# Performance work log

Measured on AMD Instinct MI355X. Metric: run time of the kernel, lower is better.

Reference implementation:

```python
import jax, jax.numpy as jnp
import numpy as np

D_CONV = 4  # matches Mamba(d_conv=4)


def _silu(v):
    return v * jax.nn.sigmoid(v)


def _mamba_block(x, in_w, cw, cb, xw, dtw, dtb, A_log, Dp, ow):
    # x: (B, L, d_model)
    B, L, _ = x.shape
    d_inner, d_state = A_log.shape
    xz = x @ in_w.T                        # (B, L, 2*d_inner)
    xr, z = jnp.split(xz, 2, axis=-1)      # each (B, L, d_inner)
    # causal depthwise conv1d (pad d_conv-1 on the left, truncate to L)
    xp = jnp.pad(xr, ((0, 0), (D_CONV - 1, 0), (0, 0)))
    xc = sum(xp[:, k:k + L, :] * cw[:, k] for k in range(D_CONV)) + cb
    xc = _silu(xc)                         # (B, L, d_inner)
    dbl = xc @ xw.T                        # (B, L, dt_rank + 2*d_state)
    dt_rank = dbl.shape[-1] - 2 * d_state
    dt, Bm, Cm = jnp.split(dbl, [dt_rank, dt_rank + d_state], axis=-1)
    dt = jax.nn.softplus(dt @ dtw.T + dtb)  # (B, L, d_inner)
    A = -jnp.exp(A_log)                    # (d_inner, d_state)
    dA = jnp.exp(dt[..., None] * A)                          # (B, L, d_inner, d_state)
    dBx = dt[..., None] * Bm[:, :, None, :] * xc[..., None]  # (B, L, d_inner, d_state)

    def step(h, inputs):
        dA_t, dBx_t, C_t = inputs          # (B,d,s), (B,d,s), (B,s)
        h = dA_t * h + dBx_t
        y = jnp.einsum('bds,bs->bd', h, C_t)
        return h, y

    h0 = jnp.zeros((B, d_inner, d_state), x.dtype)
    _, ys = jax.lax.scan(step, h0, (dA.transpose(1, 0, 2, 3),
                                    dBx.transpose(1, 0, 2, 3),
                                    Cm.transpose(1, 0, 2)))
    y = ys.transpose(1, 0, 2) + xc * Dp    # skip term D*u
    y = y * _silu(z)                       # gated
    return y @ ow.T                        # (B, L, d_model)


def setup_inputs() -> dict:
    key = jax.random.key(0)
    d_model, d_state, n_layer = 1024, 16, 2
    d_inner = 2 * d_model
    dt_rank = d_model // 16  # ceil(1024/16)
    Bsz, L = 2, 1024
    ks = jax.random.split(key, 8)
    s = 0.02
    x = jax.random.normal(ks[0], (Bsz, L, d_model), jnp.float32)
    in_proj_w = jax.random.normal(ks[1], (n_layer, 2 * d_inner, d_model), jnp.float32) * s
    conv_w = jax.random.normal(ks[2], (n_layer, d_inner, D_CONV), jnp.float32) * 0.2
    conv_b = jnp.zeros((n_layer, d_inner), jnp.float32)
    x_proj_w = jax.random.normal(ks[3], (n_layer, dt_rank + 2 * d_state, d_inner), jnp.float32) * s
    dt_proj_w = jax.random.normal(ks[4], (n_layer, d_inner, dt_rank), jnp.float32) * s
    dt_proj_b = jax.random.uniform(ks[5], (n_layer, d_inner), jnp.float32, -5.0, -3.0)
    A_log = jnp.log(jnp.tile(jnp.arange(1, d_state + 1, dtype=jnp.float32), (n_layer, d_inner, 1)))
    D = jnp.ones((n_layer, d_inner), jnp.float32)
    out_proj_w = jax.random.normal(ks[6], (n_layer, d_model, d_inner), jnp.float32) * s
    return {"x": x, "in_proj_w": in_proj_w, "conv_w": conv_w, "conv_b": conv_b,
            "x_proj_w": x_proj_w, "dt_proj_w": dt_proj_w, "dt_proj_b": dt_proj_b,
            "A_log": A_log, "D": D, "out_proj_w": out_proj_w}


def reference(x, in_proj_w, conv_w, conv_b, x_proj_w, dt_proj_w, dt_proj_b, A_log, D, out_proj_w):
    n_layer = in_proj_w.shape[0]
    for i in range(n_layer):
        x = _mamba_block(x, in_proj_w[i], conv_w[i], conv_b[i], x_proj_w[i],
                         dt_proj_w[i], dt_proj_b[i], A_log[i], D[i], out_proj_w[i])
    return x
```

## Files before the change

### kernel.cpp

```cpp
#include <hip/hip_runtime.h>
#include <hip/hip_bf16.h>
#include <cmath>

typedef __bf16 bf16x8_t __attribute__((ext_vector_type(8)));
typedef float  f32x4_t  __attribute__((ext_vector_type(4)));
using bf16 = __hip_bfloat16;

#define LOG2E 1.44269504088896340736f
#define LN2   0.69314718055994530942f

#define AS1C(p) ((const __attribute__((address_space(1))) void*)(p))
#define AS3C(p) ((__attribute__((address_space(3))) void*)(p))

__device__ __forceinline__ float fexp2(float x) { return __builtin_amdgcn_exp2f(x); }
__device__ __forceinline__ float flog2(float x) { return __builtin_amdgcn_logf(x); }
__device__ __forceinline__ float frcp (float x) { return __builtin_amdgcn_rcpf(x); }

__global__ __launch_bounds__(256)
void cast_f32_bf16(const float* __restrict__ src, bf16* __restrict__ dst, int n8)
{
    const int i = blockIdx.x * blockDim.x + threadIdx.x;
    if (i >= n8) return;
    const float4* s = (const float4*)(src + (size_t)i * 8);
    float4 a = s[0], b = s[1];
    bf16 o[8];
    o[0] = __float2bfloat16(a.x); o[1] = __float2bfloat16(a.y);
    o[2] = __float2bfloat16(a.z); o[3] = __float2bfloat16(a.w);
    o[4] = __float2bfloat16(b.x); o[5] = __float2bfloat16(b.y);
    o[6] = __float2bfloat16(b.z); o[7] = __float2bfloat16(b.w);
    *(int4*)(dst + (size_t)i * 8) = *(int4*)o;
}

template<int MODE, bool SPLITK>
__global__ __launch_bounds__(256)
void gemm_bf16(const bf16* __restrict__ A, const bf16* __restrict__ B,
               float* __restrict__ Cf, bf16* __restrict__ Cb,
               int M, int N, int K, int lda, int ldb, int ldc)
{
    __shared__ __align__(16) bf16 At[2][128][32];
    __shared__ __align__(16) bf16 Bt[2][128][32];

    const int tid  = threadIdx.x;
    const int lane = tid & 63;
    const int wid  = tid >> 6;
    const int wr   = wid >> 1;
    const int wc   = wid & 1;
    const int fr   = lane & 15;
    const int fq   = lane >> 4;

    const int row0 = blockIdx.y * 128;
    const int col0 = blockIdx.x * 128;
    const int kb   = SPLITK ? blockIdx.z * K : 0;

    const int g_row = wid * 32 + (lane >> 2);
    const int g_kp  = (lane & 3) * 8;
    const bf16* aP0 = A + (size_t)(row0 + g_row) * lda + g_kp + kb;
    const bf16* aP1 = A + (size_t)(row0 + g_row + 16) * lda + g_kp + kb;
    int bR0 = col0 + g_row;      if (bR0 >= N) bR0 = N - 1;
    int bR1 = col0 + g_row + 16; if (bR1 >= N) bR1 = N - 1;
    const bf16* bP0 = B + (size_t)bR0 * ldb + g_kp + kb;
    const bf16* bP1 = B + (size_t)bR1 * ldb + g_kp + kb;

    f32x4_t acc[4][4];
    #pragma unroll
    for (int m = 0; m < 4; ++m)
        #pragma unroll
        for (int n = 0; n < 4; ++n)
            acc[m][n] = f32x4_t{0.f, 0.f, 0.f, 0.f};

    auto STAGE = [&](int buf, int k0) {
        __builtin_amdgcn_global_load_lds(AS1C(aP0 + k0), AS3C(&At[buf][wid * 32][0]),      16, 0, 0);
        __builtin_amdgcn_global_load_lds(AS1C(aP1 + k0), AS3C(&At[buf][wid * 32 + 16][0]), 16, 0, 0);
        __builtin_amdgcn_global_load_lds(AS1C(bP0 + k0), AS3C(&Bt[buf][wid * 32][0]),      16, 0, 0);
        __builtin_amdgcn_global_load_lds(AS1C(bP1 + k0), AS3C(&Bt[buf][wid * 32 + 16][0]), 16, 0, 0);
    };

    STAGE(0, 0);
    __syncthreads();
    int cur = 0;
    for (int k0 = 0; k0 < K; k0 += 32) {
        if (k0 + 32 < K) STAGE(cur ^ 1, k0 + 32);

        bf16x8_t af[4], bg[4];
        #pragma unroll
        for (int m = 0; m < 4; ++m)
            af[m] = *(const bf16x8_t*)&At[cur][wr * 64 + m * 16 + fr][fq * 8];
        #pragma unroll
        for (int n = 0; n < 4; ++n)
            bg[n] = *(const bf16x8_t*)&Bt[cur][wc * 64 + n * 16 + fr][fq * 8];
        #pragma unroll
        for (int m = 0; m < 4; ++m)
            #pragma unroll
            for (int n = 0; n < 4; ++n)
                acc[m][n] = __builtin_amdgcn_mfma_f32_16x16x32_bf16(
                    af[m], bg[n], acc[m][n], 0, 0, 0);

        __syncthreads();
        cur ^= 1;
    }

    float* Cfz = SPLITK ? (Cf + (size_t)blockIdx.z * M * ldc) : Cf;

    #pragma unroll
    for (int m = 0; m < 4; ++m) {
        #pragma unroll
        for (int n = 0; n < 4; ++n) {
            const int c = col0 + wc * 64 + n * 16 + fr;
            if (c < N) {
                #pragma unroll
                for (int r = 0; r < 4; ++r) {
                    const int rr = row0 + wr * 64 + m * 16 + fq * 4 + r;
                    if (SPLITK || MODE != 1) Cfz[(size_t)rr * ldc + c] = acc[m][n][r];
                    if (!SPLITK && MODE != 0) Cb[(size_t)rr * ldc + c] = __float2bfloat16(acc[m][n][r]);
                }
            }
        }
    }
}

__global__ __launch_bounds__(256)
void reduce_pk(const float* __restrict__ part, float* __restrict__ of,
               bf16* __restrict__ oh, int n4, int stride4, int S)
{
    const int i = blockIdx.x * blockDim.x + threadIdx.x;
    if (i >= n4) return;
    const float4* p4 = (const float4*)part;
    float4 s = p4[i];
    for (int k = 1; k < S; ++k) {
        float4 v = p4[(size_t)k * stride4 + i];
        s.x += v.x; s.y += v.y; s.z += v.z; s.w += v.w;
    }
    if (of) ((float4*)of)[i] = s;
    if (oh) {
        bf16 o[4];
        o[0] = __float2bfloat16(s.x); o[1] = __float2bfloat16(s.y);
        o[2] = __float2bfloat16(s.z); o[3] = __float2bfloat16(s.w);
        *(int2*)(oh + (size_t)i * 4) = *(int2*)o;
    }
}

__global__ __launch_bounds__(256)
void conv_silu(const float* __restrict__ xz, const float* __restrict__ cw,
               const float* __restrict__ cb, bf16* __restrict__ xc,
               int Bsz, int L, int dinner)
{
    const int nv = dinner / 4;
    const int g  = blockIdx.x * blockDim.x + threadIdx.x;
    const int d4 = (g % nv) * 4;
    const int t  = (g / nv) % L;
    const int b  = g / (nv * L);
    if (b >= Bsz) return;

    const int ldxz = 2 * dinner;
    float4 w0 = *(const float4*)(cw + (size_t)(d4 + 0) * 4);
    float4 w1 = *(const float4*)(cw + (size_t)(d4 + 1) * 4);
    float4 w2 = *(const float4*)(cw + (size_t)(d4 + 2) * 4);
    float4 w3 = *(const float4*)(cw + (size_t)(d4 + 3) * 4);
    float4 acc = *(const float4*)(cb + d4);

    const float* base = xz + (size_t)b * L * ldxz + d4;
    #pragma unroll
    for (int k = 0; k < 4; ++k) {
        const int ts = t - 3 + k;
        if (ts >= 0) {
            float4 v = *(const float4*)(base + (size_t)ts * ldxz);
            acc.x = fmaf(v.x, (&w0.x)[k], acc.x);
            acc.y = fmaf(v.y, (&w1.x)[k], acc.y);
            acc.z = fmaf(v.z, (&w2.x)[k], acc.z);
            acc.w = fmaf(v.w, (&w3.x)[k], acc.w);
        }
    }
    acc.x = acc.x * frcp(1.f + fexp2(-acc.x * LOG2E));
    acc.y = acc.y * frcp(1.f + fexp2(-acc.y * LOG2E));
    acc.z = acc.z * frcp(1.f + fexp2(-acc.z * LOG2E));
    acc.w = acc.w * frcp(1.f + fexp2(-acc.w * LOG2E));

    bf16 o[4];
    o[0] = __float2bfloat16(acc.x); o[1] = __float2bfloat16(acc.y);
    o[2] = __float2bfloat16(acc.z); o[3] = __float2bfloat16(acc.w);
    *(int2*)(xc + ((size_t)b * L + t) * dinner + d4) = *(int2*)o;
}

__global__ __launch_bounds__(256)
void scan_part1(const bf16* __restrict__ dtraw, const bf16* __restrict__ xc,
                const float* __restrict__ dbl, const float* __restrict__ dtb,
                const float* __restrict__ alog, float* __restrict__ hend,
                float* __restrict__ Ssum, int Bsz, int L, int dinner,
                int NC, int CL)
{
    const int g  = blockIdx.x * blockDim.x + threadIdx.x;
    const int sq = g & 3;
    const int d  = (g >> 2) % dinner;
    const int c  = ((g >> 2) / dinner) % NC;
    const int b  = g / (4 * dinner * NC);
    if (b >= Bsz) return;

    float4 av = *(const float4*)(alog + (size_t)d * 16 + sq * 4);
    const float As0 = -fexp2(av.x * LOG2E) * LOG2E;
    const float As1 = -fexp2(av.y * LOG2E) * LOG2E;
    const float As2 = -fexp2(av.z * LOG2E) * LOG2E;
    const float As3 = -fexp2(av.w * LOG2E) * LOG2E;
    const float bias = dtb[d];

    const int t0 = c * CL;
    const bf16*  dt_p = dtraw + ((size_t)b * L + t0) * dinner + d;
    const bf16*  xc_p = xc    + ((size_t)b * L + t0) * dinner + d;
    const float* bl_p = dbl   + ((size_t)b * L + t0) * 96 + 64 + sq * 4;

    float h0 = 0.f, h1 = 0.f, h2 = 0.f, h3 = 0.f, S = 0.f;
    for (int t = 0; t < CL; ++t) {
        const float dtv = __bfloat162float(*dt_p);
        const float xcv = __bfloat162float(*xc_p);
        const float4 Bv = *(const float4*)bl_p;

        const float xv = dtv + bias;
        const float e  = fexp2(xv * LOG2E);
        const float sp = (xv > 15.f) ? xv : LN2 * flog2(1.f + e);
        S += sp;
        const float u = sp * xcv;
        h0 = fmaf(fexp2(sp * As0), h0, u * Bv.x);
        h1 = fmaf(fexp2(sp * As1), h1, u * Bv.y);
        h2 = fmaf(fexp2(sp * As2), h2, u * Bv.z);
        h3 = fmaf(fexp2(sp * As3), h3, u * Bv.w);

        dt_p += dinner; xc_p += dinner; bl_p += 96;
    }

    const size_t idx = ((size_t)b * NC + c) * dinner + d;
    *(float4*)(hend + idx * 16 + sq * 4) = make_float4(h0, h1, h2, h3);
    if (sq == 0) Ssum[idx] = S;
}

__global__ __launch_bounds__(256)
void chunk_prefix(float* __restrict__ hend, const float* __restrict__ Ssum,
                  const float* __restrict__ alog, int Bsz, int dinner, int NC)
{
    const int g = blockIdx.x * blockDim.x + threadIdx.x;
    const int s = g & 15;
    const int d = (g >> 4) % dinner;
    const int b = g / (16 * dinner);
    if (b >= Bsz) return;

    const float As2 = -fexp2(alog[(size_t)d * 16 + s] * LOG2E) * LOG2E;

    float h = 0.f;
    for (int c = 0; c < NC; ++c) {
        const size_t idx = ((size_t)b * NC + c) * dinner + d;
        const float he = hend[idx * 16 + s];
        const float Sv = Ssum[idx];
        hend[idx * 16 + s] = h;
        h = fmaf(fexp2(As2 * Sv), h, he);
    }
}

__global__ __launch_bounds__(256)
void scan_part2(bf16* dty, const bf16* __restrict__ xc,
                const float* __restrict__ dbl, const float* __restrict__ xz,
                const float* __restrict__ dtb, const float* __restrict__ alog,
                const float* __restrict__ Dp, const float* __restrict__ hinit,
                int Bsz, int L, int dinner, int NC, int CL)
{
    const int g  = blockIdx.x * blockDim.x + threadIdx.x;
    const int sq = g & 3;
    const int d  = (g >> 2) % dinner;
    const int c  = ((g >> 2) / dinner) % NC;
    const int b  = g / (4 * dinner * NC);
    if (b >= Bsz) return;

    float4 av = *(const float4*)(alog + (size_t)d * 16 + sq * 4);
    const float As0 = -fexp2(av.x * LOG2E) * LOG2E;
    const float As1 = -fexp2(av.y * LOG2E) * LOG2E;
    const float As2 = -fexp2(av.z * LOG2E) * LOG2E;
    const float As3 = -fexp2(av.w * LOG2E) * LOG2E;
    const float bias = dtb[d];
    const float Dval = Dp[d];

    const size_t cidx = ((size_t)b * NC + c) * dinner + d;
    float4 hv = *(const float4*)(hinit + cidx * 16 + sq * 4);
    float h0 = hv.x, h1 = hv.y, h2 = hv.z, h3 = hv.w;

    const int t0 = c * CL;
    bf16*        dt_p = dty + ((size_t)b * L + t0) * dinner + d;
    const bf16*  xc_p = xc  + ((size_t)b * L + t0) * dinner + d;
    const float* bl_p = dbl + ((size_t)b * L + t0) * 96 + 64 + sq * 4;
    const float* z_p  = xz  + ((size_t)b * L + t0) * (2 * dinner) + dinner + d;

    for (int t = 0; t < CL; ++t) {
        const float dtv = __bfloat162float(*dt_p);
        const float xcv = __bfloat162float(*xc_p);
        const float4 Bv = *(const float4*)bl_p;
        const float4 Cv = *(const float4*)(bl_p + 16);
        const float zv  = *z_p;

        const float xv = dtv + bias;
        const float e  = fexp2(xv * LOG2E);
        const float sp = (xv > 15.f) ? xv : LN2 * flog2(1.f + e);
        const float u = sp * xcv;
        h0 = fmaf(fexp2(sp * As0), h0, u * Bv.x);
        h1 = fmaf(fexp2(sp * As1), h1, u * Bv.y);
        h2 = fmaf(fexp2(sp * As2), h2, u * Bv.z);
        h3 = fmaf(fexp2(sp * As3), h3, u * Bv.w);

        float y = h0 * Cv.x + h1 * Cv.y + h2 * Cv.z + h3 * Cv.w;
        y += __shfl_xor(y, 1, 4);
        y += __shfl_xor(y, 2, 4);

        if (sq == 0) {
            y = fmaf(xcv, Dval, y);
            const float sig = frcp(1.f + fexp2(-zv * LOG2E));
            *dt_p = __float2bfloat16(y * (zv * sig));
        }

        dt_p += dinner; xc_p += dinner; bl_p += 96; z_p += 2 * dinner;
    }
}

extern "C" void kernel_launch(void* const* d_in, const int* in_sizes, int n_in,
                              void* d_out, int out_size, void* d_ws, size_t ws_size,
                              hipStream_t stream)
{
    const float* x    = (const float*)d_in[0];
    const float* inw  = (const float*)d_in[1];
    const float* cw   = (const float*)d_in[2];
    const float* cb   = (const float*)d_in[3];
    const float* xw   = (const float*)d_in[4];
    const float* dtw  = (const float*)d_in[5];
    const float* dtb  = (const float*)d_in[6];
    const float* alog = (const float*)d_in[7];
    const float* Dp   = (const float*)d_in[8];
    const float* ow   = (const float*)d_in[9];
    float* out = (float*)d_out;

    const int Bsz = 2, L = 1024, dmodel = 1024, dinner = 2048;
    const int BL = Bsz * L;
    const int NC = 32, CL = L / NC;
    const int SPX = 8,  KSX = dinner / SPX;
    const int SPO = 2,  KSO = dinner / SPO;

    char* p = (char*)d_ws;
    auto alloc = [&](size_t bytes) { char* r = p; p += (bytes + 63) & ~size_t(63); return r; };
    bf16*  wb_in  = (bf16*) alloc((size_t)2 * 2 * dinner * dmodel * 2);
    bf16*  wb_x   = (bf16*) alloc((size_t)2 * 96 * dinner * 2);
    bf16*  wb_dt  = (bf16*) alloc((size_t)2 * dinner * 64 * 2);
    bf16*  wb_ow  = (bf16*) alloc((size_t)2 * dmodel * dinner * 2);
    bf16*  curb   = (bf16*) alloc((size_t)BL * dmodel * 2);
    float* xzb    = (float*)alloc((size_t)BL * 2 * dinner * 4);
    bf16*  xcb16  = (bf16*) alloc((size_t)BL * dinner * 2);
    float* dblb   = (float*)alloc((size_t)BL * 96 * 4);
    bf16*  dblb16 = (bf16*) alloc((size_t)BL * 96 * 2);
    bf16*  dtrb16 = (bf16*) alloc((size_t)BL * dinner * 2);
    float* hendb  = (float*)alloc((size_t)Bsz * NC * dinner * 16 * 4);
    float* ssumb  = (float*)alloc((size_t)Bsz * NC * dinner * 4);
    float* partb  = (float*)alloc((size_t)SPO * BL * dmodel * 4);

    const int scan_blocks = (Bsz * NC * dinner * 4) / 256;
    const int pfx_blocks  = (Bsz * dinner * 16) / 256;

    cast_f32_bf16<<<(BL * dmodel / 8) / 256, 256, 0, stream>>>(x, curb, BL * dmodel / 8);
    cast_f32_bf16<<<(2 * 2 * dinner * dmodel / 8) / 256, 256, 0, stream>>>(
        inw, wb_in, 2 * 2 * dinner * dmodel / 8);
    cast_f32_bf16<<<(2 * 96 * dinner / 8) / 256, 256, 0, stream>>>(
        xw, wb_x, 2 * 96 * dinner / 8);
    cast_f32_bf16<<<(2 * dinner * 64 / 8) / 256, 256, 0, stream>>>(
        dtw, wb_dt, 2 * dinner * 64 / 8);
    cast_f32_bf16<<<(2 * dmodel * dinner / 8) / 256, 256, 0, stream>>>(
        ow, wb_ow, 2 * dmodel * dinner / 8);

    for (int l = 0; l < 2; ++l) {
        const bf16*  wb_in_l = wb_in + (size_t)l * 2 * dinner * dmodel;
        const bf16*  wb_x_l  = wb_x  + (size_t)l * 96 * dinner;
        const bf16*  wb_dt_l = wb_dt + (size_t)l * dinner * 64;
        const bf16*  wb_ow_l = wb_ow + (size_t)l * dmodel * dinner;
        const float* cw_l    = cw   + (size_t)l * dinner * 4;
        const float* cb_l    = cb   + (size_t)l * dinner;
        const float* dtb_l   = dtb  + (size_t)l * dinner;
        const float* alog_l  = alog + (size_t)l * dinner * 16;
        const float* Dp_l    = Dp   + (size_t)l * dinner;

        gemm_bf16<0, false><<<dim3(2 * dinner / 128, BL / 128), 256, 0, stream>>>(
            curb, wb_in_l, xzb, nullptr, BL, 2 * dinner, dmodel, dmodel, dmodel, 2 * dinner);

        conv_silu<<<(BL * dinner / 4) / 256, 256, 0, stream>>>(
            xzb, cw_l, cb_l, xcb16, Bsz, L, dinner);

        gemm_bf16<0, true><<<dim3(1, BL / 128, SPX), 256, 0, stream>>>(
            xcb16, wb_x_l, partb, nullptr, BL, 96, KSX, dinner, dinner, 96);
        reduce_pk<<<(BL * 96 / 4 + 255) / 256, 256, 0, stream>>>(
            partb, dblb, dblb16, BL * 96 / 4, BL * 96 / 4, SPX);

        gemm_bf16<1, false><<<dim3(dinner / 128, BL / 128), 256, 0, stream>>>(
            dblb16, wb_dt_l, nullptr, dtrb16, BL, dinner, 64, 96, 64, dinner);

        scan_part1<<<scan_blocks, 256, 0, stream>>>(
            dtrb16, xcb16, dblb, dtb_l, alog_l, hendb, ssumb, Bsz, L, dinner, NC, CL);
        chunk_prefix<<<pfx_blocks, 256, 0, stream>>>(
            hendb, ssumb, alog_l, Bsz, dinner, NC);
        scan_part2<<<scan_blocks, 256, 0, stream>>>(
            dtrb16, xcb16, dblb, xzb, dtb_l, alog_l, Dp_l, hendb,
            Bsz, L, dinner, NC, CL);

        gemm_bf16<0, true><<<dim3(dmodel / 128, BL / 128, SPO), 256, 0, stream>>>(
            dtrb16, wb_ow_l, partb, nullptr, BL, dmodel, KSO, dinner, dinner, dmodel);
        if (l == 0)
            reduce_pk<<<(BL * dmodel / 4 + 255) / 256, 256, 0, stream>>>(
                partb, nullptr, curb, BL * dmodel / 4, BL * dmodel / 4, SPO);
        else
            reduce_pk<<<(BL * dmodel / 4 + 255) / 256, 256, 0, stream>>>(
                partb, out, nullptr, BL * dmodel / 4, BL * dmodel / 4, SPO);
    }
}
```

Baseline: 343.0 us.

## Store xz in bf16, fuse casts, fold chunk prefix into scan, raise split-K

```diff
diff --git a/kernel.cpp b/kernel.cpp
--- a/kernel.cpp
+++ b/kernel.cpp
@@ -17,10 +17,21 @@
 __device__ __forceinline__ float frcp (float x) { return __builtin_amdgcn_rcpf(x); }
 
 __global__ __launch_bounds__(256)
-void cast_f32_bf16(const float* __restrict__ src, bf16* __restrict__ dst, int n8)
-{
-    const int i = blockIdx.x * blockDim.x + threadIdx.x;
-    if (i >= n8) return;
+void cast_multi(const float* s0, bf16* d0, int e0,
+                const float* s1, bf16* d1, int e1,
+                const float* s2, bf16* d2, int e2,
+                const float* s3, bf16* d3, int e3,
+                const float* s4, bf16* d4, int e4)
+{
+    const int blk = blockIdx.x;
+    const float* src; bf16* dst; int base;
+    if      (blk < e0) { src = s0; dst = d0; base = blk; }
+    else if (blk < e1) { src = s1; dst = d1; base = blk - e0; }
+    else if (blk < e2) { src = s2; dst = d2; base = blk - e1; }
+    else if (blk < e3) { src = s3; dst = d3; base = blk - e2; }
+    else               { src = s4; dst = d4; base = blk - e3; }
+
+    const int i = base * 256 + threadIdx.x;
     const float4* s = (const float4*)(src + (size_t)i * 8);
     float4 a = s[0], b = s[1];
     bf16 o[8];
@@ -140,7 +151,7 @@
 }
 
 __global__ __launch_bounds__(256)
-void conv_silu(const float* __restrict__ xz, const float* __restrict__ cw,
+void conv_silu(const bf16* __restrict__ xz, const float* __restrict__ cw,
                const float* __restrict__ cb, bf16* __restrict__ xc,
                int Bsz, int L, int dinner)
 {
@@ -158,16 +169,20 @@
     float4 w3 = *(const float4*)(cw + (size_t)(d4 + 3) * 4);
     float4 acc = *(const float4*)(cb + d4);
 
-    const float* base = xz + (size_t)b * L * ldxz + d4;
+    const bf16* base = xz + (size_t)b * L * ldxz + d4;
     #pragma unroll
     for (int k = 0; k < 4; ++k) {
         const int ts = t - 3 + k;
         if (ts >= 0) {
-            float4 v = *(const float4*)(base + (size_t)ts * ldxz);
-            acc.x = fmaf(v.x, (&w0.x)[k], acc.x);
-            acc.y = fmaf(v.y, (&w1.x)[k], acc.y);
-            acc.z = fmaf(v.z, (&w2.x)[k], acc.z);
-            acc.w = fmaf(v.w, (&w3.x)[k], acc.w);
+            const bf16* rp = base + (size_t)ts * ldxz;
+            float vx = __bfloat162float(rp[0]);
+            float vy = __bfloat162float(rp[1]);
+            float vz = __bfloat162float(rp[2]);
+            float vw = __bfloat162float(rp[3]);
+            acc.x = fmaf(vx, (&w0.x)[k], acc.x);
+            acc.y = fmaf(vy, (&w1.x)[k], acc.y);
+            acc.z = fmaf(vz, (&w2.x)[k], acc.z);
+            acc.w = fmaf(vw, (&w3.x)[k], acc.w);
         }
     }
     acc.x = acc.x * frcp(1.f + fexp2(-acc.x * LOG2E));
@@ -232,32 +247,11 @@
 }
 
 __global__ __launch_bounds__(256)
-void chunk_prefix(float* __restrict__ hend, const float* __restrict__ Ssum,
-                  const float* __restrict__ alog, int Bsz, int dinner, int NC)
-{
-    const int g = blockIdx.x * blockDim.x + threadIdx.x;
-    const int s = g & 15;
-    const int d = (g >> 4) % dinner;
-    const int b = g / (16 * dinner);
-    if (b >= Bsz) return;
-
-    const float As2 = -fexp2(alog[(size_t)d * 16 + s] * LOG2E) * LOG2E;
-
-    float h = 0.f;
-    for (int c = 0; c < NC; ++c) {
-        const size_t idx = ((size_t)b * NC + c) * dinner + d;
-        const float he = hend[idx * 16 + s];
-        const float Sv = Ssum[idx];
-        hend[idx * 16 + s] = h;
-        h = fmaf(fexp2(As2 * Sv), h, he);
-    }
-}
-
-__global__ __launch_bounds__(256)
 void scan_part2(bf16* dty, const bf16* __restrict__ xc,
-                const float* __restrict__ dbl, const float* __restrict__ xz,
+                const float* __restrict__ dbl, const bf16* __restrict__ xz,
                 const float* __restrict__ dtb, const float* __restrict__ alog,
-                const float* __restrict__ Dp, const float* __restrict__ hinit,
+                const float* __restrict__ Dp, const float* __restrict__ hend,
+                const float* __restrict__ Ssum,
                 int Bsz, int L, int dinner, int NC, int CL)
 {
     const int g  = blockIdx.x * blockDim.x + threadIdx.x;
@@ -275,22 +269,29 @@
     const float bias = dtb[d];
     const float Dval = Dp[d];
 
-    const size_t cidx = ((size_t)b * NC + c) * dinner + d;
-    float4 hv = *(const float4*)(hinit + cidx * 16 + sq * 4);
-    float h0 = hv.x, h1 = hv.y, h2 = hv.z, h3 = hv.w;
+    float h0 = 0.f, h1 = 0.f, h2 = 0.f, h3 = 0.f;
+    for (int cp = 0; cp < c; ++cp) {
+        const size_t idx = ((size_t)b * NC + cp) * dinner + d;
+        const float4 he = *(const float4*)(hend + idx * 16 + sq * 4);
+        const float  Sv = Ssum[idx];
+        h0 = fmaf(fexp2(As0 * Sv), h0, he.x);
+        h1 = fmaf(fexp2(As1 * Sv), h1, he.y);
+        h2 = fmaf(fexp2(As2 * Sv), h2, he.z);
+        h3 = fmaf(fexp2(As3 * Sv), h3, he.w);
+    }
 
     const int t0 = c * CL;
     bf16*        dt_p = dty + ((size_t)b * L + t0) * dinner + d;
     const bf16*  xc_p = xc  + ((size_t)b * L + t0) * dinner + d;
     const float* bl_p = dbl + ((size_t)b * L + t0) * 96 + 64 + sq * 4;
-    const float* z_p  = xz  + ((size_t)b * L + t0) * (2 * dinner) + dinner + d;
+    const bf16*  z_p  = xz  + ((size_t)b * L + t0) * (2 * dinner) + dinner + d;
 
     for (int t = 0; t < CL; ++t) {
         const float dtv = __bfloat162float(*dt_p);
         const float xcv = __bfloat162float(*xc_p);
         const float4 Bv = *(const float4*)bl_p;
         const float4 Cv = *(const float4*)(bl_p + 16);
-        const float zv  = *z_p;
+        const float zv  = __bfloat162float(*z_p);
 
         const float xv = dtv + bias;
         const float e  = fexp2(xv * LOG2E);
@@ -334,7 +335,7 @@
     const int Bsz = 2, L = 1024, dmodel = 1024, dinner = 2048;
     const int BL = Bsz * L;
     const int NC = 32, CL = L / NC;
-    const int SPX = 8,  KSX = dinner / SPX;
+    const int SPX = 16, KSX = dinner / SPX;
     const int SPO = 2,  KSO = dinner / SPO;
 
     char* p = (char*)d_ws;
@@ -344,7 +345,7 @@
     bf16*  wb_dt  = (bf16*) alloc((size_t)2 * dinner * 64 * 2);
     bf16*  wb_ow  = (bf16*) alloc((size_t)2 * dmodel * dinner * 2);
     bf16*  curb   = (bf16*) alloc((size_t)BL * dmodel * 2);
-    float* xzb    = (float*)alloc((size_t)BL * 2 * dinner * 4);
+    bf16*  xzb16  = (bf16*) alloc((size_t)BL * 2 * dinner * 2);
     bf16*  xcb16  = (bf16*) alloc((size_t)BL * dinner * 2);
     float* dblb   = (float*)alloc((size_t)BL * 96 * 4);
     bf16*  dblb16 = (bf16*) alloc((size_t)BL * 96 * 2);
@@ -354,17 +355,21 @@
     float* partb  = (float*)alloc((size_t)SPO * BL * dmodel * 4);
 
     const int scan_blocks = (Bsz * NC * dinner * 4) / 256;
-    const int pfx_blocks  = (Bsz * dinner * 16) / 256;
-
-    cast_f32_bf16<<<(BL * dmodel / 8) / 256, 256, 0, stream>>>(x, curb, BL * dmodel / 8);
-    cast_f32_bf16<<<(2 * 2 * dinner * dmodel / 8) / 256, 256, 0, stream>>>(
-        inw, wb_in, 2 * 2 * dinner * dmodel / 8);
-    cast_f32_bf16<<<(2 * 96 * dinner / 8) / 256, 256, 0, stream>>>(
-        xw, wb_x, 2 * 96 * dinner / 8);
-    cast_f32_bf16<<<(2 * dinner * 64 / 8) / 256, 256, 0, stream>>>(
-        dtw, wb_dt, 2 * dinner * 64 / 8);
-    cast_f32_bf16<<<(2 * dmodel * dinner / 8) / 256, 256, 0, stream>>>(
-        ow, wb_ow, 2 * dmodel * dinner / 8);
+
+    {
+        const int n8_x  = BL * dmodel / 8;
+        const int n8_in = 2 * 2 * dinner * dmodel / 8;
+        const int n8_xw = 2 * 96 * dinner / 8;
+        const int n8_dt = 2 * dinner * 64 / 8;
+        const int n8_ow = 2 * dmodel * dinner / 8;
+        const int e0 = n8_x / 256;
+        const int e1 = e0 + n8_in / 256;
+        const int e2 = e1 + n8_xw / 256;
+        const int e3 = e2 + n8_dt / 256;
+        const int e4 = e3 + n8_ow / 256;
+        cast_multi<<<e4, 256, 0, stream>>>(
+            x, curb, e0, inw, wb_in, e1, xw, wb_x, e2, dtw, wb_dt, e3, ow, wb_ow, e4);
+    }
 
     for (int l = 0; l < 2; ++l) {
         const bf16*  wb_in_l = wb_in + (size_t)l * 2 * dinner * dmodel;
@@ -377,11 +382,11 @@
         const float* alog_l  = alog + (size_t)l * dinner * 16;
         const float* Dp_l    = Dp   + (size_t)l * dinner;
 
-        gemm_bf16<0, false><<<dim3(2 * dinner / 128, BL / 128), 256, 0, stream>>>(
-            curb, wb_in_l, xzb, nullptr, BL, 2 * dinner, dmodel, dmodel, dmodel, 2 * dinner);
+        gemm_bf16<1, false><<<dim3(2 * dinner / 128, BL / 128), 256, 0, stream>>>(
+            curb, wb_in_l, nullptr, xzb16, BL, 2 * dinner, dmodel, dmodel, dmodel, 2 * dinner);
 
         conv_silu<<<(BL * dinner / 4) / 256, 256, 0, stream>>>(
-            xzb, cw_l, cb_l, xcb16, Bsz, L, dinner);
+            xzb16, cw_l, cb_l, xcb16, Bsz, L, dinner);
 
         gemm_bf16<0, true><<<dim3(1, BL / 128, SPX), 256, 0, stream>>>(
             xcb16, wb_x_l, partb, nullptr, BL, 96, KSX, dinner, dinner, 96);
@@ -393,10 +398,8 @@
 
         scan_part1<<<scan_blocks, 256, 0, stream>>>(
             dtrb16, xcb16, dblb, dtb_l, alog_l, hendb, ssumb, Bsz, L, dinner, NC, CL);
-        chunk_prefix<<<pfx_blocks, 256, 0, stream>>>(
-            hendb, ssumb, alog_l, Bsz, dinner, NC);
         scan_part2<<<scan_blocks, 256, 0, stream>>>(
-            dtrb16, xcb16, dblb, xzb, dtb_l, alog_l, Dp_l, hendb,
+            dtrb16, xcb16, dblb, xzb16, dtb_l, alog_l, Dp_l, hendb, ssumb,
             Bsz, L, dinner, NC, CL);
 
         gemm_bf16<0, true><<<dim3(dmodel / 128, BL / 128, SPO), 256, 0, stream>>>(
```

After: 331.4 us. 1.04x faster.
